# Performance work log

Measured on AMD Instinct MI355X. Metric: run time of the kernel, lower is better.

Reference implementation:

```python
import jax, jax.numpy as jnp
import numpy as np

LEAK = 0.01
EPS = 1e-5


def _gcn(x, W, b, src, dst, n):
    # GCNConv: add self-loops, symmetric D^-1/2 (A+I) D^-1/2 normalization
    h = x @ W
    loop = jnp.arange(n)
    s = jnp.concatenate([src, loop])
    d = jnp.concatenate([dst, loop])
    deg = jax.ops.segment_sum(jnp.ones(s.shape[0], h.dtype), d, num_segments=n)
    dinv = jnp.where(deg > 0, jax.lax.rsqrt(deg), 0.0)
    norm = dinv[s] * dinv[d]
    out = jax.ops.segment_sum(h[s] * norm[:, None], d, num_segments=n)
    return out + b


def _sage(x, Wl, bl, Wr, src, dst, n):
    # SAGEConv (mean aggr): lin_l(mean_neigh) + lin_r(x); bias on lin_l
    cnt = jax.ops.segment_sum(jnp.ones(src.shape[0], x.dtype), dst, num_segments=n)
    agg = jax.ops.segment_sum(x[src], dst, num_segments=n) / jnp.maximum(cnt, 1.0)[:, None]
    return agg @ Wl + bl + x @ Wr


def _bn(x, g, b):
    # BatchNorm over node dim, batch statistics (training forward), biased var
    m = x.mean(0)
    v = jnp.mean((x - m) ** 2, axis=0)
    return (x - m) * jax.lax.rsqrt(v + EPS) * g + b


def _lrelu(x):
    return jnp.where(x >= 0, x, LEAK * x)


def setup_inputs() -> dict:
    key = jax.random.key(0)
    ks = jax.random.split(key, 20)
    N, E, F_IN, H, G, L = 50000, 800000, 128, 128, 1000, 1000
    h2, h4, OUT = H // 2, H // 4, 32
    x = jax.random.normal(ks[0], (N, F_IN), dtype=jnp.float32)
    edge_index = jax.random.randint(ks[1], (2, E), 0, N)
    batch = jnp.sort(jax.random.randint(ks[2], (N,), 0, G))
    link_indices = jax.random.randint(ks[3], (2, L), 0, G)
    s = 0.05
    return {
        "x": x, "edge_index": edge_index, "batch": batch,
        "link_indices": link_indices, "num_graphs": G,
        "W1": jax.random.normal(ks[4], (F_IN, H), jnp.float32) * s,
        "b1": jnp.zeros((H,), jnp.float32),
        "g1": jnp.ones((H,), jnp.float32), "be1": jnp.zeros((H,), jnp.float32),
        "Wl2": jax.random.normal(ks[5], (H, h2), jnp.float32) * s,
        "bl2": jnp.zeros((h2,), jnp.float32),
        "Wr2": jax.random.normal(ks[6], (H, h2), jnp.float32) * s,
        "g2": jnp.ones((h2,), jnp.float32), "be2": jnp.zeros((h2,), jnp.float32),
        "W3": jax.random.normal(ks[7], (h2, h4), jnp.float32) * s,
        "b3": jnp.zeros((h4,), jnp.float32),
        "g3": jnp.ones((h4,), jnp.float32), "be3": jnp.zeros((h4,), jnp.float32),
        "W4": jax.random.normal(ks[8], (h4, OUT), jnp.float32) * s,
        "b4": jnp.zeros((OUT,), jnp.float32),
    }


def reference(x, edge_index, batch, link_indices, num_graphs,
              W1, b1, g1, be1, Wl2, bl2, Wr2, g2, be2,
              W3, b3, g3, be3, W4, b4):
    n = x.shape[0]
    src, dst = edge_index[0], edge_index[1]
    h = _lrelu(_bn(_gcn(x, W1, b1, src, dst, n), g1, be1))        # dropout = identity (eval)
    h = _lrelu(_bn(_sage(h, Wl2, bl2, Wr2, src, dst, n), g2, be2))
    h = _lrelu(_bn(_gcn(h, W3, b3, src, dst, n), g3, be3))
    h = _gcn(h, W4, b4, src, dst, n)
    g = jax.ops.segment_sum(h, batch, num_segments=num_graphs)     # global_add_pool
    src_emb = g[link_indices[0]]
    tgt_emb = g[link_indices[1]]
    return jax.nn.sigmoid(jnp.sum(src_emb * tgt_emb, axis=1))
```

## Files before the change

### kernel.cpp

```cpp
#include <hip/hip_runtime.h>
#include <math.h>

#define LEAK 0.01f
#define BNEPS 1e-5f
#define NCH 256
#define NGMAX 1024
#define NSLOT 64

typedef __attribute__((ext_vector_type(8))) short bf16x8;
typedef __attribute__((ext_vector_type(4))) float f32x4;
typedef __attribute__((ext_vector_type(2))) float f32x2;

__device__ inline unsigned bfpack(float a, float b) {
  unsigned ua = __float_as_uint(a);
  unsigned ub = __float_as_uint(b);
  unsigned ra = (ua + 0x7fffu + ((ua >> 16) & 1u)) >> 16;
  unsigned rb = (ub + 0x7fffu + ((ub >> 16) & 1u)) & 0xffff0000u;
  return ra | rb;
}
__device__ inline unsigned short bfround(float a) {
  unsigned ua = __float_as_uint(a);
  return (unsigned short)((ua + 0x7fffu + ((ua >> 16) & 1u)) >> 16);
}
__device__ inline float2 bfunpack(unsigned u) {
  float2 r;
  r.x = __uint_as_float(u << 16);
  r.y = __uint_as_float(u & 0xffff0000u);
  return r;
}
__device__ inline unsigned char f32_to_fp8(float v) {
  int p = __builtin_amdgcn_cvt_pk_fp8_f32(v, v, 0, false);
  return (unsigned char)(p & 0xff);
}

__global__ __launch_bounds__(256) void k_hist(const int* __restrict__ dst,
                                              int* __restrict__ H, int E, int NBK) {
  __shared__ int h[256];
  h[threadIdx.x] = 0;
  __syncthreads();
  int chunk = (E + NCH - 1) / NCH;
  int lo = blockIdx.x * chunk, hi = min(lo + chunk, E);
  for (int e = lo + threadIdx.x; e < hi; e += 256)
    atomicAdd(&h[dst[e] >> 8], 1);
  __syncthreads();
  if (threadIdx.x < NBK) H[threadIdx.x * NCH + blockIdx.x] = h[threadIdx.x];
}

__global__ __launch_bounds__(256) void k_gscan1(const int* __restrict__ in,
                                                int* __restrict__ bsum, int m) {
  int i = blockIdx.x * 256 + threadIdx.x;
  int v = (i < m) ? in[i] : 0;
#pragma unroll
  for (int s = 1; s < 64; s <<= 1) v += __shfl_xor(v, s, 64);
  __shared__ int ws[4];
  if ((threadIdx.x & 63) == 0) ws[threadIdx.x >> 6] = v;
  __syncthreads();
  if (threadIdx.x == 0) bsum[blockIdx.x] = ws[0] + ws[1] + ws[2] + ws[3];
}
__global__ __launch_bounds__(256) void k_gscan2(int* __restrict__ bsum, int NB) {
  __shared__ int lds[256];
  int t = threadIdx.x;
  int v = (t < NB) ? bsum[t] : 0;
  lds[t] = v;
  __syncthreads();
  for (int ofs = 1; ofs < 256; ofs <<= 1) {
    int u = (t >= ofs) ? lds[t - ofs] : 0;
    __syncthreads();
    lds[t] += u;
    __syncthreads();
  }
  if (t < NB) bsum[t] = lds[t] - v;
}
__global__ __launch_bounds__(256) void k_gscan3(const int* __restrict__ in,
                                                const int* __restrict__ boff,
                                                int* __restrict__ out, int m) {
  __shared__ int lds[256];
  int t = threadIdx.x;
  int i = blockIdx.x * 256 + t;
  int v = (i < m) ? in[i] : 0;
  lds[t] = v;
  __syncthreads();
  for (int ofs = 1; ofs < 256; ofs <<= 1) {
    int u = (t >= ofs) ? lds[t - ofs] : 0;
    __syncthreads();
    lds[t] += u;
    __syncthreads();
  }
  if (i < m) out[i] = boff[blockIdx.x] + lds[t] - v;
}

__global__ __launch_bounds__(256) void k_scatter_bkt(
    const int* __restrict__ src, const int* __restrict__ dst,
    const int* __restrict__ O, int* __restrict__ ebuf, int E, int NBK) {
  __shared__ int cur[256];
  if (threadIdx.x < NBK) cur[threadIdx.x] = O[threadIdx.x * NCH + blockIdx.x];
  __syncthreads();
  int chunk = (E + NCH - 1) / NCH;
  int lo = blockIdx.x * chunk, hi = min(lo + chunk, E);
  for (int e = lo + threadIdx.x; e < hi; e += 256) {
    int d = dst[e];
    int pos = atomicAdd(&cur[d >> 8], 1);
    ebuf[pos] = src[e] | ((d & 255) << 24);
  }
}

__global__ __launch_bounds__(256) void k_fill2(
    const int* __restrict__ ebuf, const int* __restrict__ O,
    int* __restrict__ eidx, int* __restrict__ rowptr,
    float* __restrict__ dinv, float* __restrict__ invcnt,
    int E, int n, int NBK) {
  __shared__ int hist[256];
  __shared__ int sc[256];
  __shared__ int cur[256];
  const int b = blockIdx.x;
  const int t = threadIdx.x;
  const int lo = O[b * NCH];
  const int hi = (b + 1 < NBK) ? O[(b + 1) * NCH] : E;
  hist[t] = 0;
  __syncthreads();
  for (int e = lo + t; e < hi; e += 256)
    atomicAdd(&hist[(ebuf[e] >> 24) & 255], 1);
  __syncthreads();
  int v = hist[t];
  sc[t] = v;
  __syncthreads();
  for (int ofs = 1; ofs < 256; ofs <<= 1) {
    int u = (t >= ofs) ? sc[t - ofs] : 0;
    __syncthreads();
    sc[t] += u;
    __syncthreads();
  }
  int excl = sc[t] - v;
  cur[t] = lo + excl;
  int node = b * 256 + t;
  if (node < n) {
    rowptr[node] = lo + excl;
    float d = (float)v;
    dinv[node]   = rsqrtf(d + 1.0f);
    invcnt[node] = 1.0f / fmaxf(d, 1.0f);
  }
  if (node == n || (b == NBK - 1 && t == 255)) rowptr[n] = E;
  __syncthreads();
  for (int e = lo + t; e < hi; e += 256) {
    int p = ebuf[e];
    int pos = atomicAdd(&cur[(p >> 24) & 255], 1);
    eidx[pos] = p & 0xFFFFFF;
  }
}

template<int F, bool FP8, bool GCN, bool ADD, bool STATS, bool POOL>
__global__ __launch_bounds__(256) void k_gather(
    const void* __restrict__ Hn, const unsigned short* __restrict__ Hbf,
    const float* __restrict__ scale,
    const int* __restrict__ rowptr, const int* __restrict__ eidx,
    const float* __restrict__ bias, const float* __restrict__ addf,
    unsigned short* __restrict__ outb,
    float* __restrict__ partials, const int* __restrict__ batch,
    float* __restrict__ gpool, int n) {
  constexpr int COLS = F / 8;
  constexpr int GPW  = 64 / COLS;
  constexpr int NPB  = 4 * GPW;
  constexpr int K    = 16 / COLS;

  const int tid  = threadIdx.x;
  const int wave = tid >> 6;
  const int lane = tid & 63;
  const int l    = lane % COLS;
  const int g    = lane / COLS;
  const int vb   = (int)blockIdx.x * NPB;
  const int v    = vb + wave * GPW + g;
  const bool valid = v < n;

  __shared__ float sred[STATS ? 2 * F : 1];
  __shared__ float pool[POOL ? NPB * 32 : 1];
  int gbase = 0;
  if constexpr (STATS) {
    if (tid < 2 * F) sred[tid] = 0.f;
  }
  if constexpr (POOL) {
    for (int i = tid; i < NPB * 32; i += 256) pool[i] = 0.f;
    gbase = batch[min(vb, n - 1)];
  }
  if constexpr (STATS || POOL) __syncthreads();

  const int lo = valid ? rowptr[v] : 0;
  const int hi = valid ? rowptr[v + 1] : 0;
  float a[8] = {0.f,0.f,0.f,0.f,0.f,0.f,0.f,0.f};

  int trips = (hi - lo + 15) >> 4;
#pragma unroll
  for (int m = 1; m < 64; m <<= 1) trips = max(trips, __shfl_xor(trips, m, 64));

  for (int bb = 0; bb < trips; bb++) {
    const int b = lo + bb * 16;
    int pre[K];
#pragma unroll
    for (int kk = 0; kk < K; kk++) {
      int e = b + l * K + kk;
      pre[kk] = (e < hi) ? eidx[e] : 0;
    }
#pragma unroll
    for (int j = 0; j < 16; j++) {
      int s = __shfl(pre[j % K], g * COLS + j / K, 64);
      if (b + j < hi) {
        if constexpr (FP8) {
          uint2 q = *(const uint2*)((const unsigned char*)Hn + (long long)s * F + l * 8);
          f32x2 p0 = __builtin_amdgcn_cvt_pk_f32_fp8(q.x, false);
          f32x2 p1 = __builtin_amdgcn_cvt_pk_f32_fp8(q.x, true);
          f32x2 p2 = __builtin_amdgcn_cvt_pk_f32_fp8(q.y, false);
          f32x2 p3 = __builtin_amdgcn_cvt_pk_f32_fp8(q.y, true);
          a[0]+=p0[0]; a[1]+=p0[1]; a[2]+=p1[0]; a[3]+=p1[1];
          a[4]+=p2[0]; a[5]+=p2[1]; a[6]+=p3[0]; a[7]+=p3[1];
        } else {
          uint4 hv = *(const uint4*)((const unsigned short*)Hn + (long long)s * F + l * 8);
          float2 p0 = bfunpack(hv.x), p1 = bfunpack(hv.y);
          float2 p2 = bfunpack(hv.z), p3 = bfunpack(hv.w);
          a[0]+=p0.x; a[1]+=p0.y; a[2]+=p1.x; a[3]+=p1.y;
          a[4]+=p2.x; a[5]+=p2.y; a[6]+=p3.x; a[7]+=p3.y;
        }
      }
    }
  }

  float o[8] = {0.f,0.f,0.f,0.f,0.f,0.f,0.f,0.f};
  if (valid) {
    float sv = scale[v];
    if constexpr (GCN) {
      uint4 hv = *(const uint4*)&Hbf[(long long)v * F + l * 8];
      float2 p0 = bfunpack(hv.x), p1 = bfunpack(hv.y);
      float2 p2 = bfunpack(hv.z), p3 = bfunpack(hv.w);
      float h[8] = {p0.x,p0.y,p1.x,p1.y,p2.x,p2.y,p3.x,p3.y};
      const float4 b0 = *(const float4*)&bias[l * 8];
      const float4 b1 = *(const float4*)&bias[l * 8 + 4];
      float bv[8] = {b0.x,b0.y,b0.z,b0.w,b1.x,b1.y,b1.z,b1.w};
#pragma unroll
      for (int j = 0; j < 8; j++) o[j] = bv[j] + sv * (a[j] + h[j]);
    } else if constexpr (ADD) {
      const float4 t0 = *(const float4*)&addf[(long long)v * F + l * 8];
      const float4 t1 = *(const float4*)&addf[(long long)v * F + l * 8 + 4];
      o[0]=fmaf(sv,a[0],t0.x); o[1]=fmaf(sv,a[1],t0.y);
      o[2]=fmaf(sv,a[2],t0.z); o[3]=fmaf(sv,a[3],t0.w);
      o[4]=fmaf(sv,a[4],t1.x); o[5]=fmaf(sv,a[5],t1.y);
      o[6]=fmaf(sv,a[6],t1.z); o[7]=fmaf(sv,a[7],t1.w);
    } else {
#pragma unroll
      for (int j = 0; j < 8; j++) o[j] = sv * a[j];
    }
    if constexpr (POOL) {
      int gi = batch[v] - gbase;
#pragma unroll
      for (int j = 0; j < 8; j++) atomicAdd(&pool[gi * 32 + l * 8 + j], o[j]);
    } else {
      uint4 u;
      u.x = bfpack(o[0], o[1]); u.y = bfpack(o[2], o[3]);
      u.z = bfpack(o[4], o[5]); u.w = bfpack(o[6], o[7]);
      *(uint4*)&outb[(long long)v * F + l * 8] = u;
    }
  }

  if constexpr (STATS) {
    if (valid) {
#pragma unroll
      for (int j = 0; j < 8; j++) {
        atomicAdd(&sred[l * 8 + j], o[j]);
        atomicAdd(&sred[F + l * 8 + j], o[j] * o[j]);
      }
    }
    __syncthreads();
    if (tid < 2 * F)
      atomicAdd(&partials[((int)blockIdx.x & (NSLOT - 1)) * 2 * F + tid], sred[tid]);
  }
  if constexpr (POOL) {
    __syncthreads();
    int vend = min(vb + NPB, n) - 1;
    int range = batch[vend] - gbase;
    int total = (range + 1) * 32;
    for (int t = tid; t < total; t += 256)
      atomicAdd(&gpool[(long long)gbase * 32 + t], pool[t]);
  }
}

template<int K, int F, bool XBF, bool BNIN, bool F8OUT>
__global__ __launch_bounds__(256) void k_gemm_mfma(
    const void* __restrict__ Xv, const float* __restrict__ W,
    const float* __restrict__ pin, const float* __restrict__ gw,
    const float* __restrict__ bw, float invN,
    const float* __restrict__ prescale,
    unsigned short* __restrict__ Yb, unsigned char* __restrict__ Yf8,
    float* __restrict__ zptr, int zcnt, int n) {
  constexpr int SP  = K + 8;
  constexpr int NCT = F / 16;
  __shared__ unsigned short sX[64 * SP];
  __shared__ unsigned short sWT[F * SP];
  __shared__ float sbn[BNIN ? 2 * K : 1];

  for (int i = blockIdx.x * 256 + threadIdx.x; i < zcnt; i += gridDim.x * 256)
    zptr[i] = 0.f;

  const int row0 = blockIdx.x * 64;
  if constexpr (BNIN) {
    int t = threadIdx.x;
    if (t < K) {
      float s1 = 0.f, s2 = 0.f;
      for (int s = 0; s < NSLOT; s++) {
        s1 += pin[s * 2 * K + t];
        s2 += pin[s * 2 * K + K + t];
      }
      float m   = s1 * invN;
      float var = s2 * invN - m * m;
      float scv = gw[t] * rsqrtf(var + BNEPS);
      sbn[t]     = scv;
      sbn[K + t] = bw[t] - m * scv;
    }
    __syncthreads();
  }
  for (int i = threadIdx.x; i < (K / 2) * F; i += 256) {
    int nn = i % F;
    int kk = (i / F) * 2;
    float w0 = W[(long long)kk * F + nn];
    float w1 = W[(long long)(kk + 1) * F + nn];
    *(unsigned*)&sWT[nn * SP + kk] = bfpack(w0, w1);
  }
  for (int i = threadIdx.x; i < 64 * (K / 8); i += 256) {
    int r = i / (K / 8), k8 = (i % (K / 8)) * 8;
    int gr = row0 + r;
    uint4 u = {0, 0, 0, 0};
    if (gr < n) {
      if constexpr (XBF) {
        const unsigned short* X = (const unsigned short*)Xv;
        uint4 raw = *(const uint4*)&X[(long long)gr * K + k8];
        if constexpr (BNIN) {
          float2 p0 = bfunpack(raw.x), p1 = bfunpack(raw.y);
          float2 p2 = bfunpack(raw.z), p3 = bfunpack(raw.w);
          float y[8] = {p0.x,p0.y,p1.x,p1.y,p2.x,p2.y,p3.x,p3.y};
#pragma unroll
          for (int j = 0; j < 8; j++) {
            float t = fmaf(y[j], sbn[k8 + j], sbn[K + k8 + j]);
            y[j] = (t >= 0.f) ? t : LEAK * t;
          }
          u.x = bfpack(y[0], y[1]); u.y = bfpack(y[2], y[3]);
          u.z = bfpack(y[4], y[5]); u.w = bfpack(y[6], y[7]);
        } else {
          u = raw;
        }
      } else {
        const float* X = (const float*)Xv;
        float4 xa = *(const float4*)&X[(long long)gr * K + k8];
        float4 xb = *(const float4*)&X[(long long)gr * K + k8 + 4];
        u.x = bfpack(xa.x, xa.y); u.y = bfpack(xa.z, xa.w);
        u.z = bfpack(xb.x, xb.y); u.w = bfpack(xb.z, xb.w);
      }
    }
    *(uint4*)&sX[r * SP + k8] = u;
  }
  __syncthreads();

  const int wv   = threadIdx.x >> 6;
  const int lane = threadIdx.x & 63;
  const int l16  = lane & 15;
  const int quad = lane >> 4;
  f32x4 acc[NCT];
#pragma unroll
  for (int c = 0; c < NCT; c++) acc[c] = (f32x4){0.f, 0.f, 0.f, 0.f};

#pragma unroll
  for (int k0 = 0; k0 < K; k0 += 32) {
    bf16x8 af = *(const bf16x8*)&sX[(wv * 16 + l16) * SP + k0 + quad * 8];
#pragma unroll
    for (int c = 0; c < NCT; c++) {
      bf16x8 bfr = *(const bf16x8*)&sWT[(c * 16 + l16) * SP + k0 + quad * 8];
      acc[c] = __builtin_amdgcn_mfma_f32_16x16x32_bf16(af, bfr, acc[c], 0, 0, 0);
    }
  }

  const int rbase = row0 + wv * 16 + quad * 4;
  float ps[4];
#pragma unroll
  for (int rg = 0; rg < 4; rg++) {
    int gr = rbase + rg;
    ps[rg] = (prescale && gr < n) ? prescale[gr] : 1.0f;
  }
#pragma unroll
  for (int c = 0; c < NCT; c++) {
    int col = c * 16 + l16;
#pragma unroll
    for (int rg = 0; rg < 4; rg++) {
      int gr = rbase + rg;
      if (gr < n) {
        float val = acc[c][rg] * ps[rg];
        Yb[(long long)gr * F + col] = bfround(val);
        if constexpr (F8OUT) Yf8[(long long)gr * F + col] = f32_to_fp8(val);
      }
    }
  }
}

__global__ __launch_bounds__(256) void k_gemm_sage_mfma(
    const unsigned short* __restrict__ X, const float* __restrict__ Wl,
    const float* __restrict__ Wr, const float* __restrict__ bl,
    const float* __restrict__ pin, const float* __restrict__ gw,
    const float* __restrict__ bw, float invN,
    unsigned char* __restrict__ t1f8, float* __restrict__ t2,
    float* __restrict__ zptr, int zcnt, int n) {
  constexpr int K = 128, F = 64, SP = K + 8, NCT = F / 16;
  __shared__ unsigned short sX[64 * SP];
  __shared__ unsigned short sWlT[F * SP];
  __shared__ unsigned short sWrT[F * SP];
  __shared__ float sbn[2 * K];

  for (int i = blockIdx.x * 256 + threadIdx.x; i < zcnt; i += gridDim.x * 256)
    zptr[i] = 0.f;

  {
    int t = threadIdx.x;
    if (t < K) {
      float s1 = 0.f, s2 = 0.f;
      for (int s = 0; s < NSLOT; s++) {
        s1 += pin[s * 2 * K + t];
        s2 += pin[s * 2 * K + K + t];
      }
      float m   = s1 * invN;
      float var = s2 * invN - m * m;
      float scv = gw[t] * rsqrtf(var + BNEPS);
      sbn[t]     = scv;
      sbn[K + t] = bw[t] - m * scv;
    }
  }
  __syncthreads();
  const int row0 = blockIdx.x * 64;
  for (int i = threadIdx.x; i < (K / 2) * F; i += 256) {
    int nn = i % F;
    int kk = (i / F) * 2;
    *(unsigned*)&sWlT[nn * SP + kk] =
        bfpack(Wl[(long long)kk * F + nn], Wl[(long long)(kk + 1) * F + nn]);
    *(unsigned*)&sWrT[nn * SP + kk] =
        bfpack(Wr[(long long)kk * F + nn], Wr[(long long)(kk + 1) * F + nn]);
  }
  for (int i = threadIdx.x; i < 64 * (K / 8); i += 256) {
    int r = i / (K / 8), k8 = (i % (K / 8)) * 8;
    int gr = row0 + r;
    uint4 u = {0, 0, 0, 0};
    if (gr < n) {
      uint4 raw = *(const uint4*)&X[(long long)gr * K + k8];
      float2 p0 = bfunpack(raw.x), p1 = bfunpack(raw.y);
      float2 p2 = bfunpack(raw.z), p3 = bfunpack(raw.w);
      float y[8] = {p0.x,p0.y,p1.x,p1.y,p2.x,p2.y,p3.x,p3.y};
#pragma unroll
      for (int j = 0; j < 8; j++) {
        float t = fmaf(y[j], sbn[k8 + j], sbn[K + k8 + j]);
        y[j] = (t >= 0.f) ? t : LEAK * t;
      }
      u.x = bfpack(y[0], y[1]); u.y = bfpack(y[2], y[3]);
      u.z = bfpack(y[4], y[5]); u.w = bfpack(y[6], y[7]);
    }
    *(uint4*)&sX[r * SP + k8] = u;
  }
  __syncthreads();

  const int wv   = threadIdx.x >> 6;
  const int lane = threadIdx.x & 63;
  const int l16  = lane & 15;
  const int quad = lane >> 4;
  f32x4 a1[NCT], a2[NCT];
#pragma unroll
  for (int c = 0; c < NCT; c++) {
    a1[c] = (f32x4){0.f, 0.f, 0.f, 0.f};
    a2[c] = (f32x4){0.f, 0.f, 0.f, 0.f};
  }
#pragma unroll
  for (int k0 = 0; k0 < K; k0 += 32) {
    bf16x8 af = *(const bf16x8*)&sX[(wv * 16 + l16) * SP + k0 + quad * 8];
#pragma unroll
    for (int c = 0; c < NCT; c++) {
      bf16x8 bl8 = *(const bf16x8*)&sWlT[(c * 16 + l16) * SP + k0 + quad * 8];
      bf16x8 br8 = *(const bf16x8*)&sWrT[(c * 16 + l16) * SP + k0 + quad * 8];
      a1[c] = __builtin_amdgcn_mfma_f32_16x16x32_bf16(af, bl8, a1[c], 0, 0, 0);
      a2[c] = __builtin_amdgcn_mfma_f32_16x16x32_bf16(af, br8, a2[c], 0, 0, 0);
    }
  }
  const int rbase = row0 + wv * 16 + quad * 4;
#pragma unroll
  for (int c = 0; c < NCT; c++) {
    int col = c * 16 + l16;
    float blv = bl[col];
#pragma unroll
    for (int rg = 0; rg < 4; rg++) {
      int gr = rbase + rg;
      if (gr < n) {
        t1f8[(long long)gr * F + col] = f32_to_fp8(a1[c][rg]);
        t2[(long long)gr * F + col]   = a2[c][rg] + blv;
      }
    }
  }
}

__global__ void k_link(const float* __restrict__ g, const int* __restrict__ li0,
                       const int* __restrict__ li1, float* __restrict__ out, int L) {
  int i = blockIdx.x * blockDim.x + threadIdx.x;
  if (i >= L) return;
  const float* a = g + (long long)li0[i] * 32;
  const float* b = g + (long long)li1[i] * 32;
  float s = 0.f;
#pragma unroll
  for (int f = 0; f < 32; f++) s = fmaf(a[f], b[f], s);
  out[i] = 1.0f / (1.0f + expf(-s));
}

extern "C" void kernel_launch(void* const* d_in, const int* in_sizes, int n_in,
                              void* d_out, int out_size, void* d_ws, size_t ws_size,
                              hipStream_t stream) {
  const float* x   = (const float*)d_in[0];
  const int* ei    = (const int*)d_in[1];
  const int* batch = (const int*)d_in[2];
  const int* li    = (const int*)d_in[3];
  const float* W1  = (const float*)d_in[5];
  const float* b1  = (const float*)d_in[6];
  const float* g1  = (const float*)d_in[7];
  const float* be1 = (const float*)d_in[8];
  const float* Wl2 = (const float*)d_in[9];
  const float* bl2 = (const float*)d_in[10];
  const float* Wr2 = (const float*)d_in[11];
  const float* g2  = (const float*)d_in[12];
  const float* be2 = (const float*)d_in[13];
  const float* W3  = (const float*)d_in[14];
  const float* b3  = (const float*)d_in[15];
  const float* g3  = (const float*)d_in[16];
  const float* be3 = (const float*)d_in[17];
  const float* W4  = (const float*)d_in[18];
  const float* b4  = (const float*)d_in[19];

  const int n = in_sizes[0] / 128;
  const int E = in_sizes[1] / 2;
  const int L = in_sizes[3] / 2;
  const int* src = ei;
  const int* dst = ei + E;
  const int* li0 = li;
  const int* li1 = li + L;
  const int NBK = (n + 255) / 256;

  char* base = (char*)d_ws;
  size_t off = 0;
  auto alloc = [&](size_t bytes) -> void* {
    void* p = (void*)(base + off);
    off = (off + bytes + 255) & ~(size_t)255;
    return p;
  };
  int*   H      = (int*)alloc((size_t)NBK * NCH * 4);
  int*   O      = (int*)alloc((size_t)NBK * NCH * 4);
  int*   hsum   = (int*)alloc((size_t)1024 * 4);
  int*   ebuf   = (int*)alloc((size_t)E * 4);
  int*   eidx   = (int*)alloc((size_t)E * 4);
  int*   rowptr = (int*)alloc((size_t)(n + 1) * 4);
  float* dinv   = (float*)alloc((size_t)n * 4);
  float* invcnt = (float*)alloc((size_t)n * 4);
  float* partials1 = (float*)alloc((size_t)NSLOT * 256 * 4);
  float* partials2 = (float*)alloc((size_t)NSLOT * 128 * 4);
  float* partials3 = (float*)alloc((size_t)NSLOT * 64 * 4);
  float* gpool  = (float*)alloc((size_t)NGMAX * 32 * 4);
  unsigned short* h1b  = (unsigned short*)alloc((size_t)n * 128 * 2);
  unsigned char*  h1f8 = (unsigned char*)alloc((size_t)n * 128);
  unsigned short* a1b  = (unsigned short*)alloc((size_t)n * 128 * 2);
  unsigned char*  t1f8 = (unsigned char*)alloc((size_t)n * 64);
  float*          t2f  = (float*)alloc((size_t)n * 64 * 4);
  unsigned short* h2b  = (unsigned short*)alloc((size_t)n * 64 * 2);
  unsigned short* h3gb = (unsigned short*)alloc((size_t)n * 32 * 2);
  unsigned short* a3b  = (unsigned short*)alloc((size_t)n * 32 * 2);
  unsigned short* h4b  = (unsigned short*)alloc((size_t)n * 32 * 2);
  (void)ws_size; (void)n_in; (void)out_size;

  const int BT = 256;
  auto cdiv = [](long long a, long long b) { return (int)((a + b - 1) / b); };
  const int GM  = cdiv(n, 64);
  const int MH  = NBK * NCH;
  const int NBH = cdiv(MH, 256);
  const float invN = 1.0f / (float)n;

  k_hist<<<NCH, 256, 0, stream>>>(dst, H, E, NBK);
  k_gscan1<<<NBH, 256, 0, stream>>>(H, hsum, MH);
  k_gscan2<<<1, 256, 0, stream>>>(hsum, NBH);
  k_gscan3<<<NBH, 256, 0, stream>>>(H, hsum, O, MH);
  k_scatter_bkt<<<NCH, 256, 0, stream>>>(src, dst, O, ebuf, E, NBK);
  k_fill2<<<NBK, 256, 0, stream>>>(ebuf, O, eidx, rowptr, dinv, invcnt, E, n, NBK);

  k_gemm_mfma<128,128,false,false,true><<<GM, 256, 0, stream>>>(
      x, W1, nullptr, nullptr, nullptr, 0.f, dinv, h1b, h1f8,
      partials1, NSLOT * 256, n);
  k_gather<128,true,true,false,true,false><<<cdiv(n,16), 256, 0, stream>>>(
      h1f8, h1b, dinv, rowptr, eidx, b1, nullptr, a1b,
      partials1, nullptr, nullptr, n);

  k_gemm_sage_mfma<<<GM, 256, 0, stream>>>(
      a1b, Wl2, Wr2, bl2, partials1, g1, be1, invN, t1f8, t2f,
      partials2, NSLOT * 128, n);
  k_gather<64,true,false,true,true,false><<<cdiv(n,32), 256, 0, stream>>>(
      t1f8, nullptr, invcnt, rowptr, eidx, nullptr, t2f, h2b,
      partials2, nullptr, nullptr, n);

  k_gemm_mfma<64,32,true,true,false><<<GM, 256, 0, stream>>>(
      h2b, W3, partials2, g2, be2, invN, dinv, h3gb, nullptr,
      partials3, NSLOT * 64, n);
  k_gather<32,false,true,false,true,false><<<cdiv(n,64), 256, 0, stream>>>(
      h3gb, h3gb, dinv, rowptr, eidx, b3, nullptr, a3b,
      partials3, nullptr, nullptr, n);

  k_gemm_mfma<32,32,true,true,false><<<GM, 256, 0, stream>>>(
      a3b, W4, partials3, g3, be3, invN, dinv, h4b, nullptr,
      gpool, NGMAX * 32, n);
  k_gather<32,false,true,false,false,true><<<cdiv(n,64), 256, 0, stream>>>(
      h4b, h4b, dinv, rowptr, eidx, b4, nullptr, nullptr,
      nullptr, batch, gpool, n);

  k_link<<<cdiv(L, BT), BT, 0, stream>>>(gpool, li0, li1, (float*)d_out, L);
}
```

Measured before the change: 393.0 us.

## Aggregate edges with balanced per-block edge-range split and shared-memory accumulators

Replaces the per-node gather kernel with an edge-balanced aggregation. Each 64-node block splits its contiguous edge range evenly among thread groups. Each group accumulates runs of same-destination edges in registers and flushes them into a shared-memory accumulator with atomics. The local node index is packed into the top bits of eidx so no rowptr search is needed, and the next neighbor row is prefetched one step ahead. This targets load imbalance and wave divergence from varying degrees, at the cost of shared atomics, a larger LDS footprint and an extra barrier.

```diff
diff --git a/kernel.cpp b/kernel.cpp
--- a/kernel.cpp
+++ b/kernel.cpp
@@ -144,12 +144,12 @@
   for (int e = lo + t; e < hi; e += 256) {
     int p = ebuf[e];
     int pos = atomicAdd(&cur[(p >> 24) & 255], 1);
-    eidx[pos] = p & 0xFFFFFF;
+    eidx[pos] = (p & 0xFFFFFF) | (((p >> 24) & 63) << 24);
   }
 }
 
 template<int F, bool FP8, bool GCN, bool ADD, bool STATS, bool POOL>
-__global__ __launch_bounds__(256) void k_gather(
+__global__ __launch_bounds__(256) void k_agg(
     const void* __restrict__ Hn, const unsigned short* __restrict__ Hbf,
     const float* __restrict__ scale,
     const int* __restrict__ rowptr, const int* __restrict__ eidx,
@@ -157,74 +157,104 @@
     unsigned short* __restrict__ outb,
     float* __restrict__ partials, const int* __restrict__ batch,
     float* __restrict__ gpool, int n) {
-  constexpr int COLS = F / 8;
-  constexpr int GPW  = 64 / COLS;
-  constexpr int NPB  = 4 * GPW;
-  constexpr int K    = 16 / COLS;
-
-  const int tid  = threadIdx.x;
-  const int wave = tid >> 6;
-  const int lane = tid & 63;
-  const int l    = lane % COLS;
-  const int g    = lane / COLS;
-  const int vb   = (int)blockIdx.x * NPB;
-  const int v    = vb + wave * GPW + g;
-  const bool valid = v < n;
-
+  constexpr int LPR  = F / 8;
+  constexpr int NG   = 256 / LPR;
+  constexpr int NN   = 64;
+  constexpr int FP   = F + 4;
+  constexpr int PMAX = 96;
+
+  __shared__ float acc[NN * FP];
   __shared__ float sred[STATS ? 2 * F : 1];
-  __shared__ float pool[POOL ? NPB * 32 : 1];
+  __shared__ float pool[POOL ? PMAX * 32 : 1];
+
+  const int tid = threadIdx.x;
+  const int l   = tid % LPR;
+  const int gid = tid / LPR;
+  const int v0  = (int)blockIdx.x * NN;
+
+  for (int i = tid; i < NN * FP; i += 256) acc[i] = 0.f;
+  if constexpr (STATS) { if (tid < 2 * F) sred[tid] = 0.f; }
   int gbase = 0;
-  if constexpr (STATS) {
-    if (tid < 2 * F) sred[tid] = 0.f;
-  }
   if constexpr (POOL) {
-    for (int i = tid; i < NPB * 32; i += 256) pool[i] = 0.f;
-    gbase = batch[min(vb, n - 1)];
-  }
-  if constexpr (STATS || POOL) __syncthreads();
-
-  const int lo = valid ? rowptr[v] : 0;
-  const int hi = valid ? rowptr[v + 1] : 0;
-  float a[8] = {0.f,0.f,0.f,0.f,0.f,0.f,0.f,0.f};
-
-  int trips = (hi - lo + 15) >> 4;
-#pragma unroll
-  for (int m = 1; m < 64; m <<= 1) trips = max(trips, __shfl_xor(trips, m, 64));
-
-  for (int bb = 0; bb < trips; bb++) {
-    const int b = lo + bb * 16;
-    int pre[K];
-#pragma unroll
-    for (int kk = 0; kk < K; kk++) {
-      int e = b + l * K + kk;
-      pre[kk] = (e < hi) ? eidx[e] : 0;
-    }
-#pragma unroll
-    for (int j = 0; j < 16; j++) {
-      int s = __shfl(pre[j % K], g * COLS + j / K, 64);
-      if (b + j < hi) {
-        if constexpr (FP8) {
-          uint2 q = *(const uint2*)((const unsigned char*)Hn + (long long)s * F + l * 8);
-          f32x2 p0 = __builtin_amdgcn_cvt_pk_f32_fp8(q.x, false);
-          f32x2 p1 = __builtin_amdgcn_cvt_pk_f32_fp8(q.x, true);
-          f32x2 p2 = __builtin_amdgcn_cvt_pk_f32_fp8(q.y, false);
-          f32x2 p3 = __builtin_amdgcn_cvt_pk_f32_fp8(q.y, true);
-          a[0]+=p0[0]; a[1]+=p0[1]; a[2]+=p1[0]; a[3]+=p1[1];
-          a[4]+=p2[0]; a[5]+=p2[1]; a[6]+=p3[0]; a[7]+=p3[1];
-        } else {
-          uint4 hv = *(const uint4*)((const unsigned short*)Hn + (long long)s * F + l * 8);
-          float2 p0 = bfunpack(hv.x), p1 = bfunpack(hv.y);
-          float2 p2 = bfunpack(hv.z), p3 = bfunpack(hv.w);
-          a[0]+=p0.x; a[1]+=p0.y; a[2]+=p1.x; a[3]+=p1.y;
-          a[4]+=p2.x; a[5]+=p2.y; a[6]+=p3.x; a[7]+=p3.y;
+    for (int i = tid; i < PMAX * 32; i += 256) pool[i] = 0.f;
+    gbase = batch[v0];
+  }
+  __syncthreads();
+
+  const int vhi  = (v0 + NN < n) ? v0 + NN : n;
+  const int elo  = rowptr[v0];
+  const int ehi  = rowptr[vhi];
+  const int span = ehi - elo;
+  const int chunk = (span + NG - 1) / NG;
+  int e = elo + gid * chunk;
+  const int ee = min(e + chunk, ehi);
+
+  float r[8] = {0.f,0.f,0.f,0.f,0.f,0.f,0.f,0.f};
+  int cur = -1;
+  int w0 = (e < ee) ? eidx[e] : 0;
+  int w1 = (e + 1 < ee) ? eidx[e + 1] : 0;
+  uint2 q2 = {0, 0};
+  uint4 q4 = {0, 0, 0, 0};
+  if (e < ee) {
+    if constexpr (FP8)
+      q2 = *(const uint2*)((const unsigned char*)Hn + (long long)(w0 & 0xFFFFFF) * F + l * 8);
+    else
+      q4 = *(const uint4*)((const unsigned short*)Hn + (long long)(w0 & 0xFFFFFF) * F + l * 8);
+  }
+
+  for (; e < ee; ++e) {
+    int w2 = (e + 2 < ee) ? eidx[e + 2] : 0;
+    uint2 n2 = {0, 0};
+    uint4 n4 = {0, 0, 0, 0};
+    if (e + 1 < ee) {
+      if constexpr (FP8)
+        n2 = *(const uint2*)((const unsigned char*)Hn + (long long)(w1 & 0xFFFFFF) * F + l * 8);
+      else
+        n4 = *(const uint4*)((const unsigned short*)Hn + (long long)(w1 & 0xFFFFFF) * F + l * 8);
+    }
+    int li = w0 >> 24;
+    if (li != cur) {
+      if (cur >= 0) {
+#pragma unroll
+        for (int j = 0; j < 8; j++) {
+          atomicAdd(&acc[cur * FP + l * 8 + j], r[j]);
+          r[j] = 0.f;
         }
       }
-    }
-  }
-
-  float o[8] = {0.f,0.f,0.f,0.f,0.f,0.f,0.f,0.f};
-  if (valid) {
+      cur = li;
+    }
+    if constexpr (FP8) {
+      f32x2 p0 = __builtin_amdgcn_cvt_pk_f32_fp8(q2.x, false);
+      f32x2 p1 = __builtin_amdgcn_cvt_pk_f32_fp8(q2.x, true);
+      f32x2 p2 = __builtin_amdgcn_cvt_pk_f32_fp8(q2.y, false);
+      f32x2 p3 = __builtin_amdgcn_cvt_pk_f32_fp8(q2.y, true);
+      r[0]+=p0[0]; r[1]+=p0[1]; r[2]+=p1[0]; r[3]+=p1[1];
+      r[4]+=p2[0]; r[5]+=p2[1]; r[6]+=p3[0]; r[7]+=p3[1];
+    } else {
+      float2 p0 = bfunpack(q4.x), p1 = bfunpack(q4.y);
+      float2 p2 = bfunpack(q4.z), p3 = bfunpack(q4.w);
+      r[0]+=p0.x; r[1]+=p0.y; r[2]+=p1.x; r[3]+=p1.y;
+      r[4]+=p2.x; r[5]+=p2.y; r[6]+=p3.x; r[7]+=p3.y;
+    }
+    w0 = w1; w1 = w2;
+    if constexpr (FP8) q2 = n2; else q4 = n4;
+  }
+  if (cur >= 0) {
+#pragma unroll
+    for (int j = 0; j < 8; j++) atomicAdd(&acc[cur * FP + l * 8 + j], r[j]);
+  }
+  __syncthreads();
+
+  float s1[8] = {0.f,0.f,0.f,0.f,0.f,0.f,0.f,0.f};
+  float s2[8] = {0.f,0.f,0.f,0.f,0.f,0.f,0.f,0.f};
+  for (int li = gid; li < NN; li += NG) {
+    int v = v0 + li;
+    if (v >= n) break;
     float sv = scale[v];
+    float av[8];
+#pragma unroll
+    for (int j = 0; j < 8; j++) av[j] = acc[li * FP + l * 8 + j];
+    float o[8];
     if constexpr (GCN) {
       uint4 hv = *(const uint4*)&Hbf[(long long)v * F + l * 8];
       float2 p0 = bfunpack(hv.x), p1 = bfunpack(hv.y);
@@ -234,22 +264,33 @@
       const float4 b1 = *(const float4*)&bias[l * 8 + 4];
       float bv[8] = {b0.x,b0.y,b0.z,b0.w,b1.x,b1.y,b1.z,b1.w};
 #pragma unroll
-      for (int j = 0; j < 8; j++) o[j] = bv[j] + sv * (a[j] + h[j]);
+      for (int j = 0; j < 8; j++) o[j] = bv[j] + sv * (av[j] + h[j]);
     } else if constexpr (ADD) {
       const float4 t0 = *(const float4*)&addf[(long long)v * F + l * 8];
       const float4 t1 = *(const float4*)&addf[(long long)v * F + l * 8 + 4];
-      o[0]=fmaf(sv,a[0],t0.x); o[1]=fmaf(sv,a[1],t0.y);
-      o[2]=fmaf(sv,a[2],t0.z); o[3]=fmaf(sv,a[3],t0.w);
-      o[4]=fmaf(sv,a[4],t1.x); o[5]=fmaf(sv,a[5],t1.y);
-      o[6]=fmaf(sv,a[6],t1.z); o[7]=fmaf(sv,a[7],t1.w);
+      o[0]=fmaf(sv,av[0],t0.x); o[1]=fmaf(sv,av[1],t0.y);
+      o[2]=fmaf(sv,av[2],t0.z); o[3]=fmaf(sv,av[3],t0.w);
+      o[4]=fmaf(sv,av[4],t1.x); o[5]=fmaf(sv,av[5],t1.y);
+      o[6]=fmaf(sv,av[6],t1.z); o[7]=fmaf(sv,av[7],t1.w);
     } else {
 #pragma unroll
-      for (int j = 0; j < 8; j++) o[j] = sv * a[j];
+      for (int j = 0; j < 8; j++) o[j] = sv * av[j];
+    }
+    if constexpr (STATS) {
+#pragma unroll
+      for (int j = 0; j < 8; j++) { s1[j] += o[j]; s2[j] += o[j] * o[j]; }
     }
     if constexpr (POOL) {
-      int gi = batch[v] - gbase;
-#pragma unroll
-      for (int j = 0; j < 8; j++) atomicAdd(&pool[gi * 32 + l * 8 + j], o[j]);
+      int gv = batch[v];
+      int gi = gv - gbase;
+      if (gi < PMAX) {
+#pragma unroll
+        for (int j = 0; j < 8; j++) atomicAdd(&pool[gi * 32 + l * 8 + j], o[j]);
+      } else {
+#pragma unroll
+        for (int j = 0; j < 8; j++)
+          atomicAdd(&gpool[(long long)gv * 32 + l * 8 + j], o[j]);
+      }
     } else {
       uint4 u;
       u.x = bfpack(o[0], o[1]); u.y = bfpack(o[2], o[3]);
@@ -257,14 +298,11 @@
       *(uint4*)&outb[(long long)v * F + l * 8] = u;
     }
   }
-
   if constexpr (STATS) {
-    if (valid) {
-#pragma unroll
-      for (int j = 0; j < 8; j++) {
-        atomicAdd(&sred[l * 8 + j], o[j]);
-        atomicAdd(&sred[F + l * 8 + j], o[j] * o[j]);
-      }
+#pragma unroll
+    for (int j = 0; j < 8; j++) {
+      atomicAdd(&sred[l * 8 + j], s1[j]);
+      atomicAdd(&sred[F + l * 8 + j], s2[j]);
     }
     __syncthreads();
     if (tid < 2 * F)
@@ -272,10 +310,10 @@
   }
   if constexpr (POOL) {
     __syncthreads();
-    int vend = min(vb + NPB, n) - 1;
+    int vend = ((v0 + NN < n) ? v0 + NN : n) - 1;
     int range = batch[vend] - gbase;
-    int total = (range + 1) * 32;
-    for (int t = tid; t < total; t += 256)
+    int lim = (range + 1 < PMAX ? range + 1 : PMAX) * 32;
+    for (int t = tid; t < lim; t += 256)
       atomicAdd(&gpool[(long long)gbase * 32 + t], pool[t]);
   }
 }
@@ -571,6 +609,7 @@
   const int BT = 256;
   auto cdiv = [](long long a, long long b) { return (int)((a + b - 1) / b); };
   const int GM  = cdiv(n, 64);
+  const int GA  = cdiv(n, 64);
   const int MH  = NBK * NCH;
   const int NBH = cdiv(MH, 256);
   const float invN = 1.0f / (float)n;
@@ -585,28 +624,28 @@
   k_gemm_mfma<128,128,false,false,true><<<GM, 256, 0, stream>>>(
       x, W1, nullptr, nullptr, nullptr, 0.f, dinv, h1b, h1f8,
       partials1, NSLOT * 256, n);
-  k_gather<128,true,true,false,true,false><<<cdiv(n,16), 256, 0, stream>>>(
+  k_agg<128,true,true,false,true,false><<<GA, 256, 0, stream>>>(
       h1f8, h1b, dinv, rowptr, eidx, b1, nullptr, a1b,
       partials1, nullptr, nullptr, n);
 
   k_gemm_sage_mfma<<<GM, 256, 0, stream>>>(
       a1b, Wl2, Wr2, bl2, partials1, g1, be1, invN, t1f8, t2f,
       partials2, NSLOT * 128, n);
-  k_gather<64,true,false,true,true,false><<<cdiv(n,32), 256, 0, stream>>>(
+  k_agg<64,true,false,true,true,false><<<GA, 256, 0, stream>>>(
       t1f8, nullptr, invcnt, rowptr, eidx, nullptr, t2f, h2b,
       partials2, nullptr, nullptr, n);
 
   k_gemm_mfma<64,32,true,true,false><<<GM, 256, 0, stream>>>(
       h2b, W3, partials2, g2, be2, invN, dinv, h3gb, nullptr,
       partials3, NSLOT * 64, n);
-  k_gather<32,false,true,false,true,false><<<cdiv(n,64), 256, 0, stream>>>(
+  k_agg<32,false,true,false,true,false><<<GA, 256, 0, stream>>>(
       h3gb, h3gb, dinv, rowptr, eidx, b3, nullptr, a3b,
       partials3, nullptr, nullptr, n);
 
   k_gemm_mfma<32,32,true,true,false><<<GM, 256, 0, stream>>>(
       a3b, W4, partials3, g3, be3, invN, dinv, h4b, nullptr,
       gpool, NGMAX * 32, n);
-  k_gather<32,false,true,false,false,true><<<cdiv(n,64), 256, 0, stream>>>(
+  k_agg<32,false,true,false,false,true><<<GA, 256, 0, stream>>>(
       h4b, h4b, dinv, rowptr, eidx, b4, nullptr, nullptr,
       nullptr, batch, gpool, n);
 
```

After: 428.1 us. +8.9%, slower.
